# Kernel optimization log

Measured on AMD Instinct MI355X. Metric: run time of the kernel, lower is better.

Reference implementation:

```python
import jax, jax.numpy as jnp
import numpy as np
import math

V, T, D, N, H, DFF = 32000, 1024, 1024, 6, 16, 4096
DK = D // H
EPS = 1e-6


def setup_inputs() -> dict:
    key = jax.random.key(0)
    ks = jax.random.split(key, 20)
    s = 0.02
    B = 2
    return {
        "idx": jax.random.randint(ks[0], (B, T), 0, V, dtype=jnp.int32),
        "emb": jax.random.normal(ks[1], (V, D), jnp.float32) * s,
        # attention projections, stored [in, out] so y = x @ W
        "Wq": jax.random.normal(ks[2], (N, D, D), jnp.float32) * s,
        "Wk": jax.random.normal(ks[3], (N, D, D), jnp.float32) * s,
        "Wv": jax.random.normal(ks[4], (N, D, D), jnp.float32) * s,
        "Wo": jax.random.normal(ks[5], (N, D, D), jnp.float32) * s,
        "ln1_a": jnp.ones((N, D), jnp.float32),
        "ln1_b": jnp.zeros((N, D), jnp.float32),
        "ln2_a": jnp.ones((N, D), jnp.float32),
        "ln2_b": jnp.zeros((N, D), jnp.float32),
        "W1": jax.random.normal(ks[6], (N, D, DFF), jnp.float32) * s,
        "b1": jnp.zeros((N, DFF), jnp.float32),
        "W2": jax.random.normal(ks[7], (N, DFF, D), jnp.float32) * s,
        "b2": jnp.zeros((N, D), jnp.float32),
        "fnorm_a": jnp.ones((D,), jnp.float32),
        "fnorm_b": jnp.zeros((D,), jnp.float32),
        "Wp": jax.random.normal(ks[8], (D, V), jnp.float32) * s,
        "bp": jnp.zeros((V,), jnp.float32),
    }


def _layernorm(x, a, b):
    # torch .std() uses Bessel correction (ddof=1); denom is (std + eps), not sqrt(var+eps)
    mean = x.mean(axis=-1, keepdims=True)
    std = jnp.std(x, axis=-1, keepdims=True, ddof=1)
    return a * (x - mean) / (std + EPS) + b


def _pos_encoding(t, d):
    pos = jnp.arange(t, dtype=jnp.float32)[:, None]
    div = jnp.exp(jnp.arange(0, d, 2, dtype=jnp.float32) * (-math.log(10000.0) / d))
    pe = jnp.zeros((t, d), jnp.float32)
    pe = pe.at[:, 0::2].set(jnp.sin(pos * div))
    pe = pe.at[:, 1::2].set(jnp.cos(pos * div))
    return pe


def _forward(idx, emb, Wq, Wk, Wv, Wo, ln1_a, ln1_b, ln2_a, ln2_b,
             W1, b1, W2, b2, fnorm_a, fnorm_b, Wp, bp):
    B, Tc = idx.shape
    x = emb[idx] * math.sqrt(D) + _pos_encoding(Tc, D)  # [B,T,D]
    causal = jnp.tril(jnp.ones((Tc, Tc), bool))  # [T,T]

    def block(x, p):
        wq, wk, wv, wo, a1, c1, a2, c2, w1, bb1, w2, bb2 = p
        h_in = _layernorm(x, a1, c1)
        q = (h_in @ wq).reshape(B, Tc, H, DK).transpose(0, 2, 1, 3)
        k = (h_in @ wk).reshape(B, Tc, H, DK).transpose(0, 2, 1, 3)
        v = (h_in @ wv).reshape(B, Tc, H, DK).transpose(0, 2, 1, 3)
        scores = jnp.einsum('bhqd,bhkd->bhqk', q, k) / math.sqrt(DK)
        scores = jnp.where(causal, scores, -1e9)
        attn = jax.nn.softmax(scores, axis=-1)
        o = jnp.einsum('bhqk,bhkd->bhqd', attn, v)
        o = o.transpose(0, 2, 1, 3).reshape(B, Tc, D) @ wo
        x = x + o
        h2 = _layernorm(x, a2, c2)
        ff = jax.nn.relu(h2 @ w1 + bb1) @ w2 + bb2
        x = x + ff
        return x, None

    x, _ = jax.lax.scan(block, x, (Wq, Wk, Wv, Wo, ln1_a, ln1_b, ln2_a, ln2_b, W1, b1, W2, b2))
    x = _layernorm(x, fnorm_a, fnorm_b)
    logits = x @ Wp + bp  # [B,T,V]
    return logits


def reference(idx, emb, Wq, Wk, Wv, Wo, ln1_a, ln1_b, ln2_a, ln2_b,
              W1, b1, W2, b2, fnorm_a, fnorm_b, Wp, bp):
    return _forward(idx, emb, Wq, Wk, Wv, Wo, ln1_a, ln1_b, ln2_a, ln2_b,
                    W1, b1, W2, b2, fnorm_a, fnorm_b, Wp, bp)
```

## Files before the change

### kernel.cpp

```cpp
#include <hip/hip_runtime.h>
#include <hip/hip_bf16.h>
#include <math.h>

#define VOCAB 32000
#define TSEQ 1024
#define DMODEL 1024
#define NLAYERS 6
#define NHEADS 16
#define DFF 4096
#define DKH 64
#define BATCH 2
#define MROWS (BATCH * TSEQ)
#define LN_EPS 1e-6f
#define QKVS 3072

typedef unsigned short u16;
typedef __attribute__((ext_vector_type(8))) short short8v;
typedef __attribute__((ext_vector_type(4))) float f32x4;

#define WAITCNT_VM(N) asm volatile("s_waitcnt vmcnt(" #N ")" ::: "memory")

__device__ __forceinline__ u16 f2bb(float f) {
    __hip_bfloat16 h = __float2bfloat16(f);
    u16 u; __builtin_memcpy(&u, &h, 2); return u;
}

__device__ __forceinline__ void gload16(const void* g, void* l) {
    __builtin_amdgcn_global_load_lds(
        (const __attribute__((address_space(1))) unsigned int*)g,
        (__attribute__((address_space(3))) unsigned int*)l, 16, 0, 0);
}

__global__ void embed_kernel(const int* __restrict__ idx,
                             const float* __restrict__ emb,
                             float* __restrict__ x) {
    int i = blockIdx.x * blockDim.x + threadIdx.x;
    if (i >= MROWS * DMODEL) return;
    int row = i / DMODEL;
    int d = i - row * DMODEL;
    int t = row % TSEQ;
    int tok = idx[row];
    float e = emb[(size_t)tok * DMODEL + d] * 32.0f;
    float freq = expf(-(float)(d & ~1) * (9.210340371976184f / (float)DMODEL));
    float ang = (float)t * freq;
    float pe = (d & 1) ? cosf(ang) : sinf(ang);
    x[i] = e + pe;
}

template<bool OB16>
__global__ void __launch_bounds__(256) ln_kernel(const float* __restrict__ x,
                                                 const float* __restrict__ a,
                                                 const float* __restrict__ b,
                                                 void* __restrict__ yv) {
    __shared__ float red[8];
    int row = blockIdx.x;
    int tid = threadIdx.x;
    float4 v = ((const float4*)(x + (size_t)row * DMODEL))[tid];
    float s = v.x + v.y + v.z + v.w;
    #pragma unroll
    for (int off = 32; off; off >>= 1) s += __shfl_xor(s, off, 64);
    if ((tid & 63) == 0) red[tid >> 6] = s;
    __syncthreads();
    float mean = (red[0] + red[1] + red[2] + red[3]) * (1.0f / DMODEL);
    float dx = v.x - mean, dy = v.y - mean, dz = v.z - mean, dw = v.w - mean;
    float ss = dx * dx + dy * dy + dz * dz + dw * dw;
    #pragma unroll
    for (int off = 32; off; off >>= 1) ss += __shfl_xor(ss, off, 64);
    if ((tid & 63) == 0) red[4 + (tid >> 6)] = ss;
    __syncthreads();
    float var = (red[4] + red[5] + red[6] + red[7]) * (1.0f / (DMODEL - 1));
    float inv = 1.0f / (sqrtf(var) + LN_EPS);
    const float4 a4 = ((const float4*)a)[tid];
    const float4 b4 = ((const float4*)b)[tid];
    float o0 = a4.x * dx * inv + b4.x;
    float o1 = a4.y * dy * inv + b4.y;
    float o2 = a4.z * dz * inv + b4.z;
    float o3 = a4.w * dw * inv + b4.w;
    if (OB16) {
        ushort4 o; o.x = f2bb(o0); o.y = f2bb(o1); o.z = f2bb(o2); o.w = f2bb(o3);
        ((ushort4*)((u16*)yv + (size_t)row * DMODEL))[tid] = o;
    } else {
        float4 o; o.x = o0; o.y = o1; o.z = o2; o.w = o3;
        ((float4*)((float*)yv + (size_t)row * DMODEL))[tid] = o;
    }
}

__global__ void __launch_bounds__(256) convT(const float* __restrict__ in,
                                             u16* __restrict__ out, int K, int N) {
    __shared__ float t[32][33];
    in  += (size_t)blockIdx.z * K * N;
    out += (size_t)blockIdx.z * K * N;
    const int tx = threadIdx.x, ty = threadIdx.y;
    const int n0 = blockIdx.x * 32, k0 = blockIdx.y * 32;
    #pragma unroll
    for (int i = 0; i < 4; ++i)
        t[ty + i * 8][tx] = in[(size_t)(k0 + ty + i * 8) * N + n0 + tx];
    __syncthreads();
    #pragma unroll
    for (int i = 0; i < 4; ++i)
        out[(size_t)(n0 + ty + i * 8) * K + k0 + tx] = f2bb(t[tx][ty + i * 8]);
}

__global__ void __launch_bounds__(256) convQKVO(const float* __restrict__ Wq,
                                                const float* __restrict__ Wk,
                                                const float* __restrict__ Wv,
                                                const float* __restrict__ Wo,
                                                u16* __restrict__ WqkvT,
                                                u16* __restrict__ WoT) {
    __shared__ float t[32][33];
    const int z = blockIdx.z, L = z >> 2, p = z & 3;
    const size_t MM = (size_t)DMODEL * DMODEL;
    const float* in = (p == 0 ? Wq : p == 1 ? Wk : p == 2 ? Wv : Wo) + (size_t)L * MM;
    u16* out = (p < 3) ? (WqkvT + (size_t)L * 3 * MM + (size_t)p * MM)
                       : (WoT + (size_t)L * MM);
    const int tx = threadIdx.x, ty = threadIdx.y;
    const int n0 = blockIdx.x * 32, k0 = blockIdx.y * 32;
    #pragma unroll
    for (int i = 0; i < 4; ++i)
        t[ty + i * 8][tx] = in[(size_t)(k0 + ty + i * 8) * DMODEL + n0 + tx];
    __syncthreads();
    #pragma unroll
    for (int i = 0; i < 4; ++i)
        out[(size_t)(n0 + ty + i * 8) * DMODEL + k0 + tx] = f2bb(t[tx][ty + i * 8]);
}

template<int BMT, int WAVES, bool BIAS, bool RELU, bool RES, bool OB16>
__global__ void __launch_bounds__(WAVES * 64) gemm_mfma(
    const u16* __restrict__ A, const u16* __restrict__ Bt,
    const float* __restrict__ bias, const float* res,
    void* outp, int N, int K)
{
    constexpr int WROWS = BMT / (WAVES / 2);
    constexpr int MR = WROWS / 16;
    constexpr int SR = WAVES * 16;
    constexpr int AR = BMT / SR;
    constexpr int BR = 128 / SR;
    constexpr int LD = AR + BR;
    __shared__ u16 Alds[3][BMT * 32];
    __shared__ u16 Blds[3][128 * 32];
    const int tid = threadIdx.x;
    const int w = tid >> 6, lane = tid & 63;
    const int wr = w >> 1, wc = w & 1;
    const size_t bm = (size_t)blockIdx.y * BMT;
    const size_t bn = (size_t)blockIdx.x * 128;
    const int srow = (w << 4) + (lane >> 2);
    const int scol = (((lane & 3) ^ ((lane >> 3) & 3)) << 3);
    const int fr = lane & 15, fq = lane >> 4;
    const int aswz = ((fq ^ ((fr >> 1) & 3)) << 3);

    f32x4 acc[MR][4];
    #pragma unroll
    for (int m = 0; m < MR; ++m)
        #pragma unroll
        for (int n = 0; n < 4; ++n)
            acc[m][n] = (f32x4){0.f, 0.f, 0.f, 0.f};

    auto issue = [&](int kt, int buf) {
        const int k0 = kt * 32;
        #pragma unroll
        for (int li = 0; li < AR; ++li)
            gload16(A + (bm + li * SR + srow) * K + k0 + scol,
                    Alds[buf] + li * (SR * 32) + w * 512);
        #pragma unroll
        for (int li = 0; li < BR; ++li)
            gload16(Bt + (bn + li * SR + srow) * K + k0 + scol,
                    Blds[buf] + li * (SR * 32) + w * 512);
    };

    const int nt = K / 32;
    issue(0, 0);
    issue(1, 1);
    if constexpr (LD == 4) WAITCNT_VM(4); else WAITCNT_VM(3);
    __builtin_amdgcn_s_barrier();
    __builtin_amdgcn_sched_barrier(0);

    for (int t = 0; t < nt; ++t) {
        const int pf = (t + 2 < nt) ? t + 2 : nt - 1;
        issue(pf, (t + 2) % 3);
        if constexpr (LD == 4) WAITCNT_VM(8); else WAITCNT_VM(6);
        __builtin_amdgcn_s_barrier();
        __builtin_amdgcn_sched_barrier(0);
        const u16* Ab = Alds[t % 3];
        const u16* Bb = Blds[t % 3];
        short8v a[MR], b[4];
        #pragma unroll
        for (int m = 0; m < MR; ++m)
            a[m] = *(const short8v*)(Ab + (wr * WROWS + m * 16 + fr) * 32 + aswz);
        #pragma unroll
        for (int n = 0; n < 4; ++n)
            b[n] = *(const short8v*)(Bb + (wc * 64 + n * 16 + fr) * 32 + aswz);
        #pragma unroll
        for (int m = 0; m < MR; ++m)
            #pragma unroll
            for (int n = 0; n < 4; ++n)
                acc[m][n] = __builtin_amdgcn_mfma_f32_16x16x32_bf16(a[m], b[n], acc[m][n], 0, 0, 0);
        __builtin_amdgcn_s_barrier();
    }
    WAITCNT_VM(0);

    #pragma unroll
    for (int n = 0; n < 4; ++n) {
        const size_t col = bn + wc * 64 + n * 16 + fr;
        const float bv = BIAS ? bias[col] : 0.f;
        #pragma unroll
        for (int m = 0; m < MR; ++m) {
            #pragma unroll
            for (int r = 0; r < 4; ++r) {
                const size_t row = bm + wr * WROWS + m * 16 + fq * 4 + r;
                float v = acc[m][n][r] + bv;
                if (RELU) v = fmaxf(v, 0.f);
                if (RES)  v += res[row * N + col];
                if (OB16) ((u16*)outp)[row * N + col] = f2bb(v);
                else      ((float*)outp)[row * N + col] = v;
            }
        }
    }
}

__global__ void __launch_bounds__(256) attn_flash(const u16* __restrict__ qkv,
                                                  u16* __restrict__ o) {
    __shared__ u16 Klds[64 * 64];
    __shared__ u16 Vt[64 * 64];
    __shared__ u16 Plds[4][16 * 72];

    const int tid = threadIdx.x;
    const int w = tid >> 6, lane = tid & 63;
    const int fr = lane & 15, fq = lane >> 4;
    const int qt = gridDim.x - 1 - blockIdx.x;
    const int h = blockIdx.y, b = blockIdx.z;
    const int qbase = qt * 64 + w * 16;
    const size_t rowbase = (size_t)b * TSEQ;
    const int hd = h * DKH;

    const int rk = tid >> 3;
    const int c8 = (tid & 7) << 3;

    const u16* qrow = qkv + (rowbase + qbase + fr) * QKVS + hd;
    const short8v qf0 = *(const short8v*)(qrow + fq * 8);
    const short8v qf1 = *(const short8v*)(qrow + 32 + fq * 8);

    float m[4], l[4];
    f32x4 oa[4];
    #pragma unroll
    for (int r = 0; r < 4; ++r) { m[r] = -1e30f; l[r] = 0.f; }
    #pragma unroll
    for (int nd = 0; nd < 4; ++nd) oa[nd] = (f32x4){0.f, 0.f, 0.f, 0.f};

    short8v ka0, ka1, va0, va1;
    short8v kb0, kb1, vb0, vb1;

    auto load_set = [&](int j0, short8v& k0v, short8v& k1v, short8v& v0v, short8v& v1v) {
        const size_t gk = (rowbase + j0 + rk) * QKVS + hd + c8 + 1024;
        k0v = *(const short8v*)(qkv + gk);
        k1v = *(const short8v*)(qkv + gk + (size_t)32 * QKVS);
        const size_t gv = (rowbase + j0 + 2 * rk) * QKVS + hd + c8 + 2048;
        v0v = *(const short8v*)(qkv + gv);
        v1v = *(const short8v*)(qkv + gv + QKVS);
    };
    auto stage_set = [&](const short8v& k0v, const short8v& k1v,
                         const short8v& v0v, const short8v& v1v) {
        const int kb0b = (rk * 128 + c8 * 2) ^ ((rk & 7) << 4);
        *(short8v*)((char*)Klds + kb0b) = k0v;
        const int r2 = rk + 32;
        const int kb1b = (r2 * 128 + c8 * 2) ^ ((r2 & 7) << 4);
        *(short8v*)((char*)Klds + kb1b) = k1v;
        #pragma unroll
        for (int i = 0; i < 8; ++i) {
            const int vrow = c8 + i;
            const int slot = (((2 * rk) >> 3) + (vrow >> 3)) & 7;
            unsigned int pair = ((unsigned int)(u16)v0v[i]) |
                                (((unsigned int)(u16)v1v[i]) << 16);
            *(unsigned int*)(&Vt[vrow * 64 + slot * 8 + ((2 * rk) & 7)]) = pair;
        }
    };
    auto do_tile = [&](int t) {
        const int j0 = t * 64;
        f32x4 s[4];
        __builtin_amdgcn_s_setprio(1);
        #pragma unroll
        for (int ct = 0; ct < 4; ++ct) {
            const int krow = ct * 16 + fr;
            const int swz = (krow & 7) << 4;
            short8v k0 = *(const short8v*)((char*)Klds + ((krow * 128 + fq * 16) ^ swz));
            short8v k1 = *(const short8v*)((char*)Klds + ((krow * 128 + 64 + fq * 16) ^ swz));
            f32x4 a = (f32x4){0.f, 0.f, 0.f, 0.f};
            a = __builtin_amdgcn_mfma_f32_16x16x32_bf16(qf0, k0, a, 0, 0, 0);
            a = __builtin_amdgcn_mfma_f32_16x16x32_bf16(qf1, k1, a, 0, 0, 0);
            s[ct] = a;
        }
        __builtin_amdgcn_s_setprio(0);

        float c[4];
        #pragma unroll
        for (int r = 0; r < 4; ++r) {
            const int qg = qbase + fq * 4 + r;
            float sv[4];
            #pragma unroll
            for (int ct = 0; ct < 4; ++ct) {
                sv[ct] = s[ct][r] * 0.125f;
                if (j0 + ct * 16 + fr > qg) sv[ct] = -1e30f;
            }
            float mx = fmaxf(fmaxf(sv[0], sv[1]), fmaxf(sv[2], sv[3]));
            mx = fmaxf(mx, __shfl_xor(mx, 1, 64));
            mx = fmaxf(mx, __shfl_xor(mx, 2, 64));
            mx = fmaxf(mx, __shfl_xor(mx, 4, 64));
            mx = fmaxf(mx, __shfl_xor(mx, 8, 64));
            const float mn = fmaxf(m[r], mx);
            c[r] = __expf(m[r] - mn);
            m[r] = mn;
            float p0 = __expf(sv[0] - mn);
            float p1 = __expf(sv[1] - mn);
            float p2 = __expf(sv[2] - mn);
            float p3 = __expf(sv[3] - mn);
            float rs = (p0 + p1) + (p2 + p3);
            rs += __shfl_xor(rs, 1, 64);
            rs += __shfl_xor(rs, 2, 64);
            rs += __shfl_xor(rs, 4, 64);
            rs += __shfl_xor(rs, 8, 64);
            l[r] = l[r] * c[r] + rs;
            u16* prow = &Plds[w][(fq * 4 + r) * 72];
            prow[fr]      = f2bb(p0);
            prow[16 + fr] = f2bb(p1);
            prow[32 + fr] = f2bb(p2);
            prow[48 + fr] = f2bb(p3);
        }
        #pragma unroll
        for (int nd = 0; nd < 4; ++nd)
            #pragma unroll
            for (int r = 0; r < 4; ++r)
                oa[nd][r] *= c[r];
        asm volatile("s_waitcnt lgkmcnt(0)" ::: "memory");
        __builtin_amdgcn_sched_barrier(0);

        __builtin_amdgcn_s_setprio(1);
        #pragma unroll
        for (int ks = 0; ks < 2; ++ks) {
            const short8v pf = *(const short8v*)(&Plds[w][fr * 72 + ks * 32 + fq * 8]);
            #pragma unroll
            for (int nd = 0; nd < 4; ++nd) {
                const int vrow = nd * 16 + fr;
                const int slot = (ks * 4 + fq + (vrow >> 3)) & 7;
                const short8v vf = *(const short8v*)(&Vt[vrow * 64 + slot * 8]);
                oa[nd] = __builtin_amdgcn_mfma_f32_16x16x32_bf16(pf, vf, oa[nd], 0, 0, 0);
            }
        }
        __builtin_amdgcn_s_setprio(0);
    };

    load_set(0, ka0, ka1, va0, va1);
    int t = 0;
    for (;;) {
        stage_set(ka0, ka1, va0, va1);
        __syncthreads();
        if (t < qt) load_set((t + 1) * 64, kb0, kb1, vb0, vb1);
        do_tile(t);
        __syncthreads();
        if (++t > qt) break;
        stage_set(kb0, kb1, vb0, vb1);
        __syncthreads();
        if (t < qt) load_set((t + 1) * 64, ka0, ka1, va0, va1);
        do_tile(t);
        __syncthreads();
        if (++t > qt) break;
    }

    #pragma unroll
    for (int r = 0; r < 4; ++r) {
        const float inv = 1.0f / l[r];
        u16* orow = o + (rowbase + qbase + fq * 4 + r) * DMODEL + hd;
        #pragma unroll
        for (int nd = 0; nd < 4; ++nd)
            orow[nd * 16 + fr] = f2bb(oa[nd][r] * inv);
    }
}

#define FBM 64
#define FBN 64
#define FBK 16
__global__ void __launch_bounds__(256) gemm_f32(
    const float* __restrict__ A, const float* __restrict__ Bw,
    const float* __restrict__ bias, float* outp, int N, int K)
{
    __shared__ float As[FBK][FBM];
    __shared__ float Bs[FBK][FBN];
    const int bm = blockIdx.y * FBM, bn = blockIdx.x * FBN;
    const int tid = threadIdx.x;
    const int tr = (tid >> 4) << 2, tc = (tid & 15) << 2;
    const int am = tid >> 2, ak = (tid & 3) << 2;
    const int bk = tid >> 4, bn4 = (tid & 15) << 2;
    float acc[4][4] = {};
    const float* Ap = A + (size_t)(bm + am) * K + ak;
    const float* Bp = Bw + (size_t)bk * N + bn + bn4;
    for (int k0 = 0; k0 < K; k0 += FBK) {
        float4 av = *(const float4*)(Ap + k0);
        float4 bv = *(const float4*)(Bp + (size_t)k0 * N);
        As[ak + 0][am] = av.x; As[ak + 1][am] = av.y; As[ak + 2][am] = av.z; As[ak + 3][am] = av.w;
        *(float4*)&Bs[bk][bn4] = bv;
        __syncthreads();
        #pragma unroll
        for (int kk = 0; kk < FBK; ++kk) {
            float4 a4 = *(const float4*)&As[kk][tr];
            float4 b4 = *(const float4*)&Bs[kk][tc];
            acc[0][0] += a4.x*b4.x; acc[0][1] += a4.x*b4.y; acc[0][2] += a4.x*b4.z; acc[0][3] += a4.x*b4.w;
            acc[1][0] += a4.y*b4.x; acc[1][1] += a4.y*b4.y; acc[1][2] += a4.y*b4.z; acc[1][3] += a4.y*b4.w;
            acc[2][0] += a4.z*b4.x; acc[2][1] += a4.z*b4.y; acc[2][2] += a4.z*b4.z; acc[2][3] += a4.z*b4.w;
            acc[3][0] += a4.w*b4.x; acc[3][1] += a4.w*b4.y; acc[3][2] += a4.w*b4.z; acc[3][3] += a4.w*b4.w;
        }
        __syncthreads();
    }
    #pragma unroll
    for (int i = 0; i < 4; ++i) {
        int row = bm + tr + i;
        float4 o;
        o.x = acc[i][0] + bias[bn + tc + 0];
        o.y = acc[i][1] + bias[bn + tc + 1];
        o.z = acc[i][2] + bias[bn + tc + 2];
        o.w = acc[i][3] + bias[bn + tc + 3];
        *(float4*)(outp + (size_t)row * N + bn + tc) = o;
    }
}

extern "C" void kernel_launch(void* const* d_in, const int* in_sizes, int n_in,
                              void* d_out, int out_size, void* d_ws, size_t ws_size,
                              hipStream_t stream) {
    const int* idx = (const int*)d_in[0];
    const float* emb = (const float*)d_in[1];
    const float* Wq = (const float*)d_in[2];
    const float* Wk = (const float*)d_in[3];
    const float* Wv = (const float*)d_in[4];
    const float* Wo = (const float*)d_in[5];
    const float* ln1a = (const float*)d_in[6];
    const float* ln1b = (const float*)d_in[7];
    const float* ln2a = (const float*)d_in[8];
    const float* ln2b = (const float*)d_in[9];
    const float* W1 = (const float*)d_in[10];
    const float* b1 = (const float*)d_in[11];
    const float* W2 = (const float*)d_in[12];
    const float* b2 = (const float*)d_in[13];
    const float* fa = (const float*)d_in[14];
    const float* fb = (const float*)d_in[15];
    const float* Wp = (const float*)d_in[16];
    const float* bp = (const float*)d_in[17];
    float* out = (float*)d_out;

    const size_t MD = (size_t)MROWS * DMODEL;
    const size_t MM = (size_t)DMODEL * DMODEL;
    u16* U = (u16*)out;
    u16* qkv = U;
    u16* ob = U + 3 * MD;
    u16* hb = U + 4 * MD;
    float* x = (float*)(U + 5 * MD);
    u16* ff = U + 7 * MD;
    u16* WqkvT = U + 12 * MD;
    u16* WoT = U + 21 * MD;
    u16* W1T = U + 24 * MD;
    u16* W2T = U + 36 * MD;

    const bool pathA = ws_size >= (size_t)68 * 1024 * 1024 + 256;
    u16* WpT = (u16*)d_ws;
    u16* h2b = (u16*)((char*)d_ws + (size_t)64 * 1024 * 1024);
    float* hF = (float*)d_ws;

    dim3 cblk(32, 8);
    convQKVO<<<dim3(32, 32, 24), cblk, 0, stream>>>(Wq, Wk, Wv, Wo, WqkvT, WoT);
    convT<<<dim3(128, 32, 6), cblk, 0, stream>>>(W1, W1T, DMODEL, DFF);
    convT<<<dim3(32, 128, 6), cblk, 0, stream>>>(W2, W2T, DFF, DMODEL);
    if (pathA) convT<<<dim3(1000, 32, 1), cblk, 0, stream>>>(Wp, WpT, DMODEL, VOCAB);

    embed_kernel<<<(MROWS * DMODEL + 255) / 256, 256, 0, stream>>>(idx, emb, x);

    for (int L = 0; L < NLAYERS; ++L) {
        ln_kernel<true><<<MROWS, 256, 0, stream>>>(x, ln1a + (size_t)L * DMODEL, ln1b + (size_t)L * DMODEL, hb);
        gemm_mfma<128, 4, false, false, false, true><<<dim3(24, 16), 256, 0, stream>>>(
            hb, WqkvT + (size_t)L * 3 * MM, nullptr, nullptr, qkv, QKVS, DMODEL);
        attn_flash<<<dim3(TSEQ / 64, NHEADS, BATCH), 256, 0, stream>>>(qkv, ob);
        gemm_mfma<64, 4, false, false, true, false><<<dim3(8, 32), 256, 0, stream>>>(
            ob, WoT + (size_t)L * MM, nullptr, x, x, DMODEL, DMODEL);
        ln_kernel<true><<<MROWS, 256, 0, stream>>>(x, ln2a + (size_t)L * DMODEL, ln2b + (size_t)L * DMODEL, hb);
        gemm_mfma<256, 8, true, true, false, true><<<dim3(32, 8), 512, 0, stream>>>(
            hb, W1T + (size_t)L * DFF * DMODEL, b1 + (size_t)L * DFF, nullptr, ff, DFF, DMODEL);
        gemm_mfma<64, 4, true, false, true, false><<<dim3(8, 32), 256, 0, stream>>>(
            ff, W2T + (size_t)L * DFF * DMODEL, b2 + (size_t)L * DMODEL, x, x, DMODEL, DFF);
    }

    if (pathA) {
        ln_kernel<true><<<MROWS, 256, 0, stream>>>(x, fa, fb, h2b);
        gemm_mfma<256, 8, true, false, false, false><<<dim3(250, 8), 512, 0, stream>>>(
            h2b, WpT, bp, nullptr, out, VOCAB, DMODEL);
    } else {
        ln_kernel<false><<<MROWS, 256, 0, stream>>>(x, fa, fb, hF);
        gemm_f32<<<dim3(VOCAB / FBN, MROWS / FBM), 256, 0, stream>>>(hF, Wp, bp, out, VOCAB, DMODEL);
    }
}
```

Measured before the change: 1.643 ms.

## Enlarge attention query tile to 128 rows with 8 waves per block

The flash-attention kernel now processes 128 query rows per block with 512 threads (8 waves), so each staged K/V tile in shared memory is reused by twice as many query rows. Each thread now loads one K row and one V row per tile, and waves whose queries lie entirely before a key tile skip its compute. This halves the grid (256 blocks) and adds per-wave causal imbalance: the early waves sit idle on diagonal tiles and the number of resident blocks shrinks, which can reduce the latency hiding available.

```diff
diff --git a/kernel.cpp b/kernel.cpp
--- a/kernel.cpp
+++ b/kernel.cpp
@@ -217,22 +217,22 @@
     }
 }
 
-__global__ void __launch_bounds__(256) attn_flash(const u16* __restrict__ qkv,
+__global__ void __launch_bounds__(512) attn_flash(const u16* __restrict__ qkv,
                                                   u16* __restrict__ o) {
     __shared__ u16 Klds[64 * 64];
     __shared__ u16 Vt[64 * 64];
-    __shared__ u16 Plds[4][16 * 72];
+    __shared__ u16 Plds[8][16 * 72];
 
     const int tid = threadIdx.x;
     const int w = tid >> 6, lane = tid & 63;
     const int fr = lane & 15, fq = lane >> 4;
     const int qt = gridDim.x - 1 - blockIdx.x;
     const int h = blockIdx.y, b = blockIdx.z;
-    const int qbase = qt * 64 + w * 16;
+    const int qbase = qt * 128 + w * 16;
     const size_t rowbase = (size_t)b * TSEQ;
     const int hd = h * DKH;
 
-    const int rk = tid >> 3;
+    const int r = tid >> 3;
     const int c8 = (tid & 7) << 3;
 
     const u16* qrow = qkv + (rowbase + qbase + fr) * QKVS + hd;
@@ -242,135 +242,129 @@
     float m[4], l[4];
     f32x4 oa[4];
     #pragma unroll
-    for (int r = 0; r < 4; ++r) { m[r] = -1e30f; l[r] = 0.f; }
+    for (int rr = 0; rr < 4; ++rr) { m[rr] = -1e30f; l[rr] = 0.f; }
     #pragma unroll
     for (int nd = 0; nd < 4; ++nd) oa[nd] = (f32x4){0.f, 0.f, 0.f, 0.f};
 
-    short8v ka0, ka1, va0, va1;
-    short8v kb0, kb1, vb0, vb1;
-
-    auto load_set = [&](int j0, short8v& k0v, short8v& k1v, short8v& v0v, short8v& v1v) {
-        const size_t gk = (rowbase + j0 + rk) * QKVS + hd + c8 + 1024;
-        k0v = *(const short8v*)(qkv + gk);
-        k1v = *(const short8v*)(qkv + gk + (size_t)32 * QKVS);
-        const size_t gv = (rowbase + j0 + 2 * rk) * QKVS + hd + c8 + 2048;
-        v0v = *(const short8v*)(qkv + gv);
-        v1v = *(const short8v*)(qkv + gv + QKVS);
+    short8v ka, va;
+    short8v kb, vb;
+
+    auto load_set = [&](int j0, short8v& kv, short8v& vv) {
+        const size_t g = (rowbase + j0 + r) * QKVS + hd + c8;
+        kv = *(const short8v*)(qkv + g + 1024);
+        vv = *(const short8v*)(qkv + g + 2048);
     };
-    auto stage_set = [&](const short8v& k0v, const short8v& k1v,
-                         const short8v& v0v, const short8v& v1v) {
-        const int kb0b = (rk * 128 + c8 * 2) ^ ((rk & 7) << 4);
-        *(short8v*)((char*)Klds + kb0b) = k0v;
-        const int r2 = rk + 32;
-        const int kb1b = (r2 * 128 + c8 * 2) ^ ((r2 & 7) << 4);
-        *(short8v*)((char*)Klds + kb1b) = k1v;
+    auto stage_set = [&](const short8v& kv, const short8v& vv) {
+        const int kb_b = (r * 128 + c8 * 2) ^ ((r & 7) << 4);
+        *(short8v*)((char*)Klds + kb_b) = kv;
         #pragma unroll
         for (int i = 0; i < 8; ++i) {
             const int vrow = c8 + i;
-            const int slot = (((2 * rk) >> 3) + (vrow >> 3)) & 7;
-            unsigned int pair = ((unsigned int)(u16)v0v[i]) |
-                                (((unsigned int)(u16)v1v[i]) << 16);
-            *(unsigned int*)(&Vt[vrow * 64 + slot * 8 + ((2 * rk) & 7)]) = pair;
+            const int slot = ((r >> 3) + (vrow >> 3)) & 7;
+            Vt[vrow * 64 + slot * 8 + (r & 7)] = (u16)vv[i];
         }
     };
     auto do_tile = [&](int t) {
         const int j0 = t * 64;
-        f32x4 s[4];
-        __builtin_amdgcn_s_setprio(1);
-        #pragma unroll
-        for (int ct = 0; ct < 4; ++ct) {
-            const int krow = ct * 16 + fr;
-            const int swz = (krow & 7) << 4;
-            short8v k0 = *(const short8v*)((char*)Klds + ((krow * 128 + fq * 16) ^ swz));
-            short8v k1 = *(const short8v*)((char*)Klds + ((krow * 128 + 64 + fq * 16) ^ swz));
-            f32x4 a = (f32x4){0.f, 0.f, 0.f, 0.f};
-            a = __builtin_amdgcn_mfma_f32_16x16x32_bf16(qf0, k0, a, 0, 0, 0);
-            a = __builtin_amdgcn_mfma_f32_16x16x32_bf16(qf1, k1, a, 0, 0, 0);
-            s[ct] = a;
+        if (j0 <= qbase + 15) {
+            f32x4 s[4];
+            __builtin_amdgcn_s_setprio(1);
+            #pragma unroll
+            for (int ct = 0; ct < 4; ++ct) {
+                const int krow = ct * 16 + fr;
+                const int swz = (krow & 7) << 4;
+                short8v k0 = *(const short8v*)((char*)Klds + ((krow * 128 + fq * 16) ^ swz));
+                short8v k1 = *(const short8v*)((char*)Klds + ((krow * 128 + 64 + fq * 16) ^ swz));
+                f32x4 a = (f32x4){0.f, 0.f, 0.f, 0.f};
+                a = __builtin_amdgcn_mfma_f32_16x16x32_bf16(qf0, k0, a, 0, 0, 0);
+                a = __builtin_amdgcn_mfma_f32_16x16x32_bf16(qf1, k1, a, 0, 0, 0);
+                s[ct] = a;
+            }
+            __builtin_amdgcn_s_setprio(0);
+
+            float c[4];
+            #pragma unroll
+            for (int rr = 0; rr < 4; ++rr) {
+                const int qg = qbase + fq * 4 + rr;
+                float sv[4];
+                #pragma unroll
+                for (int ct = 0; ct < 4; ++ct) {
+                    sv[ct] = s[ct][rr] * 0.125f;
+                    if (j0 + ct * 16 + fr > qg) sv[ct] = -1e30f;
+                }
+                float mx = fmaxf(fmaxf(sv[0], sv[1]), fmaxf(sv[2], sv[3]));
+                mx = fmaxf(mx, __shfl_xor(mx, 1, 64));
+                mx = fmaxf(mx, __shfl_xor(mx, 2, 64));
+                mx = fmaxf(mx, __shfl_xor(mx, 4, 64));
+                mx = fmaxf(mx, __shfl_xor(mx, 8, 64));
+                const float mn = fmaxf(m[rr], mx);
+                c[rr] = __expf(m[rr] - mn);
+                m[rr] = mn;
+                float p0 = __expf(sv[0] - mn);
+                float p1 = __expf(sv[1] - mn);
+                float p2 = __expf(sv[2] - mn);
+                float p3 = __expf(sv[3] - mn);
+                float rs = (p0 + p1) + (p2 + p3);
+                rs += __shfl_xor(rs, 1, 64);
+                rs += __shfl_xor(rs, 2, 64);
+                rs += __shfl_xor(rs, 4, 64);
+                rs += __shfl_xor(rs, 8, 64);
+                l[rr] = l[rr] * c[rr] + rs;
+                u16* prow = &Plds[w][(fq * 4 + rr) * 72];
+                prow[fr]      = f2bb(p0);
+                prow[16 + fr] = f2bb(p1);
+                prow[32 + fr] = f2bb(p2);
+                prow[48 + fr] = f2bb(p3);
+            }
+            #pragma unroll
+            for (int nd = 0; nd < 4; ++nd)
+                #pragma unroll
+                for (int rr = 0; rr < 4; ++rr)
+                    oa[nd][rr] *= c[rr];
+            asm volatile("s_waitcnt lgkmcnt(0)" ::: "memory");
+            __builtin_amdgcn_sched_barrier(0);
+
+            __builtin_amdgcn_s_setprio(1);
+            #pragma unroll
+            for (int ks = 0; ks < 2; ++ks) {
+                const short8v pfv = *(const short8v*)(&Plds[w][fr * 72 + ks * 32 + fq * 8]);
+                #pragma unroll
+                for (int nd = 0; nd < 4; ++nd) {
+                    const int vrow = nd * 16 + fr;
+                    const int slot = (ks * 4 + fq + (vrow >> 3)) & 7;
+                    const short8v vf = *(const short8v*)(&Vt[vrow * 64 + slot * 8]);
+                    oa[nd] = __builtin_amdgcn_mfma_f32_16x16x32_bf16(pfv, vf, oa[nd], 0, 0, 0);
+                }
+            }
+            __builtin_amdgcn_s_setprio(0);
         }
-        __builtin_amdgcn_s_setprio(0);
-
-        float c[4];
-        #pragma unroll
-        for (int r = 0; r < 4; ++r) {
-            const int qg = qbase + fq * 4 + r;
-            float sv[4];
-            #pragma unroll
-            for (int ct = 0; ct < 4; ++ct) {
-                sv[ct] = s[ct][r] * 0.125f;
-                if (j0 + ct * 16 + fr > qg) sv[ct] = -1e30f;
-            }
-            float mx = fmaxf(fmaxf(sv[0], sv[1]), fmaxf(sv[2], sv[3]));
-            mx = fmaxf(mx, __shfl_xor(mx, 1, 64));
-            mx = fmaxf(mx, __shfl_xor(mx, 2, 64));
-            mx = fmaxf(mx, __shfl_xor(mx, 4, 64));
-            mx = fmaxf(mx, __shfl_xor(mx, 8, 64));
-            const float mn = fmaxf(m[r], mx);
-            c[r] = __expf(m[r] - mn);
-            m[r] = mn;
-            float p0 = __expf(sv[0] - mn);
-            float p1 = __expf(sv[1] - mn);
-            float p2 = __expf(sv[2] - mn);
-            float p3 = __expf(sv[3] - mn);
-            float rs = (p0 + p1) + (p2 + p3);
-            rs += __shfl_xor(rs, 1, 64);
-            rs += __shfl_xor(rs, 2, 64);
-            rs += __shfl_xor(rs, 4, 64);
-            rs += __shfl_xor(rs, 8, 64);
-            l[r] = l[r] * c[r] + rs;
-            u16* prow = &Plds[w][(fq * 4 + r) * 72];
-            prow[fr]      = f2bb(p0);
-            prow[16 + fr] = f2bb(p1);
-            prow[32 + fr] = f2bb(p2);
-            prow[48 + fr] = f2bb(p3);
-        }
-        #pragma unroll
-        for (int nd = 0; nd < 4; ++nd)
-            #pragma unroll
-            for (int r = 0; r < 4; ++r)
-                oa[nd][r] *= c[r];
-        asm volatile("s_waitcnt lgkmcnt(0)" ::: "memory");
-        __builtin_amdgcn_sched_barrier(0);
-
-        __builtin_amdgcn_s_setprio(1);
-        #pragma unroll
-        for (int ks = 0; ks < 2; ++ks) {
-            const short8v pf = *(const short8v*)(&Plds[w][fr * 72 + ks * 32 + fq * 8]);
-            #pragma unroll
-            for (int nd = 0; nd < 4; ++nd) {
-                const int vrow = nd * 16 + fr;
-                const int slot = (ks * 4 + fq + (vrow >> 3)) & 7;
-                const short8v vf = *(const short8v*)(&Vt[vrow * 64 + slot * 8]);
-                oa[nd] = __builtin_amdgcn_mfma_f32_16x16x32_bf16(pf, vf, oa[nd], 0, 0, 0);
-            }
-        }
-        __builtin_amdgcn_s_setprio(0);
     };
 
-    load_set(0, ka0, ka1, va0, va1);
+    const int ntiles = 2 * qt + 2;
+    load_set(0, ka, va);
     int t = 0;
     for (;;) {
-        stage_set(ka0, ka1, va0, va1);
-        __syncthreads();
-        if (t < qt) load_set((t + 1) * 64, kb0, kb1, vb0, vb1);
+        stage_set(ka, va);
+        __syncthreads();
+        if (t + 1 < ntiles) load_set((t + 1) * 64, kb, vb);
         do_tile(t);
         __syncthreads();
-        if (++t > qt) break;
-        stage_set(kb0, kb1, vb0, vb1);
-        __syncthreads();
-        if (t < qt) load_set((t + 1) * 64, ka0, ka1, va0, va1);
+        if (++t >= ntiles) break;
+        stage_set(kb, vb);
+        __syncthreads();
+        if (t + 1 < ntiles) load_set((t + 1) * 64, ka, va);
         do_tile(t);
         __syncthreads();
-        if (++t > qt) break;
-    }
-
-    #pragma unroll
-    for (int r = 0; r < 4; ++r) {
-        const float inv = 1.0f / l[r];
-        u16* orow = o + (rowbase + qbase + fq * 4 + r) * DMODEL + hd;
+        if (++t >= ntiles) break;
+    }
+
+    #pragma unroll
+    for (int rr = 0; rr < 4; ++rr) {
+        const float inv = 1.0f / l[rr];
+        u16* orow = o + (rowbase + qbase + fq * 4 + rr) * DMODEL + hd;
         #pragma unroll
         for (int nd = 0; nd < 4; ++nd)
-            orow[nd * 16 + fr] = f2bb(oa[nd][r] * inv);
+            orow[nd * 16 + fr] = f2bb(oa[nd][rr] * inv);
     }
 }
 
@@ -473,7 +467,7 @@
         ln_kernel<true><<<MROWS, 256, 0, stream>>>(x, ln1a + (size_t)L * DMODEL, ln1b + (size_t)L * DMODEL, hb);
         gemm_mfma<128, 4, false, false, false, true><<<dim3(24, 16), 256, 0, stream>>>(
             hb, WqkvT + (size_t)L * 3 * MM, nullptr, nullptr, qkv, QKVS, DMODEL);
-        attn_flash<<<dim3(TSEQ / 64, NHEADS, BATCH), 256, 0, stream>>>(qkv, ob);
+        attn_flash<<<dim3(TSEQ / 128, NHEADS, BATCH), 512, 0, stream>>>(qkv, ob);
         gemm_mfma<64, 4, false, false, true, false><<<dim3(8, 32), 256, 0, stream>>>(
             ob, WoT + (size_t)L * MM, nullptr, x, x, DMODEL, DMODEL);
         ln_kernel<true><<<MROWS, 256, 0, stream>>>(x, ln2a + (size_t)L * DMODEL, ln2b + (size_t)L * DMODEL, hb);
```

Result: no change. 1.637 ms (-0.4%).
